# Kernel tuning notes

Measured on AMD Instinct MI355X. Metric: run time of the kernel, lower is better.

Reference implementation:

```python
import jax, jax.numpy as jnp
import numpy as np

E = 2          # n_modalities
HQ = 16        # n_heads
HK = 8         # n_kv_heads
HD = 128       # head_dim
DIM = 2048
BS = 2
SEQ = 2048
EPS = 1e-6
ROPE_THETA = 10000.0


def _rmsnorm(x, w):
    # x: (..., d), w broadcastable to x
    return x * jax.lax.rsqrt(jnp.mean(x * x, axis=-1, keepdims=True) + EPS) * w


def _apply_rope(t, cos, sin):
    # t: (bs, seq, H, HD); cos/sin: (seq, HD//2). Complex rotation on pairs.
    t2 = t.reshape(*t.shape[:-1], HD // 2, 2)
    t0, t1 = t2[..., 0], t2[..., 1]
    c = cos[None, :, None, :]
    s = sin[None, :, None, :]
    out = jnp.stack([t0 * c - t1 * s, t0 * s + t1 * c], axis=-1)
    return out.reshape(t.shape)


def setup_inputs() -> dict:
    key = jax.random.key(0)
    ks = jax.random.split(key, 8)
    pos = jnp.arange(SEQ, dtype=jnp.float32)
    inv_freq = 1.0 / (ROPE_THETA ** (jnp.arange(0, HD, 2, dtype=jnp.float32) / HD))
    ang = pos[:, None] * inv_freq[None, :]  # (SEQ, HD//2)
    return {
        "x": jax.random.normal(ks[0], (BS, SEQ, DIM), jnp.float32),
        "freqs_cos": jnp.cos(ang),
        "freqs_sin": jnp.sin(ang),
        "wq": jax.random.normal(ks[1], (E, DIM, HQ * HD), jnp.float32) * 0.02,
        "wk": jax.random.normal(ks[2], (E, DIM, HK * HD), jnp.float32) * 0.02,
        "wv": jax.random.normal(ks[3], (E, DIM, HK * HD), jnp.float32) * 0.02,
        "wo": jax.random.normal(ks[4], (E, HQ * HD, DIM), jnp.float32) * 0.02,
        "q_norm_w": jnp.ones((E, HD), jnp.float32),
        "k_norm_w": jnp.ones((E, HD), jnp.float32),
        "attn_norm_w": jnp.ones((E, DIM), jnp.float32),
        "modality_ids": jax.random.randint(ks[5], (BS * SEQ,), 0, E, jnp.int32),
    }


def reference(x, freqs_cos, freqs_sin, wq, wk, wv, wo,
              q_norm_w, k_norm_w, attn_norm_w, modality_ids):
    bs, seq, dim = x.shape
    xf = x.reshape(-1, dim)  # (N, dim)
    onehot = (modality_ids[None, :] == jnp.arange(E, dtype=modality_ids.dtype)[:, None]).astype(x.dtype)  # (E, N)

    # Per-modality QKV projections + QK RMSNorm, then combine by modality id
    q = jnp.einsum('nd,edh->enh', xf, wq).reshape(E, -1, HQ, HD)
    q = _rmsnorm(q, q_norm_w[:, None, None, :])
    q = jnp.einsum('en,enhd->nhd', onehot, q).reshape(bs, seq, HQ, HD)

    k = jnp.einsum('nd,edh->enh', xf, wk).reshape(E, -1, HK, HD)
    k = _rmsnorm(k, k_norm_w[:, None, None, :])
    k = jnp.einsum('en,enhd->nhd', onehot, k).reshape(bs, seq, HK, HD)

    v = jnp.einsum('nd,edh->enh', xf, wv).reshape(E, -1, HK, HD)
    v = jnp.einsum('en,enhd->nhd', onehot, v).reshape(bs, seq, HK, HD)

    # RoPE
    q = _apply_rope(q, freqs_cos, freqs_sin)
    k = _apply_rope(k, freqs_cos, freqs_sin)

    # repeat_kv for GQA
    n_rep = HQ // HK
    k = jnp.repeat(k, n_rep, axis=2)
    v = jnp.repeat(v, n_rep, axis=2)

    # Global causal SDPA
    qh = jnp.swapaxes(q, 1, 2)  # (bs, HQ, seq, HD)
    kh = jnp.swapaxes(k, 1, 2)
    vh = jnp.swapaxes(v, 1, 2)
    scores = jnp.einsum('bhqd,bhkd->bhqk', qh, kh) / jnp.sqrt(jnp.asarray(HD, x.dtype))
    causal = jnp.tril(jnp.ones((seq, seq), dtype=bool))
    scores = jnp.where(causal[None, None], scores, jnp.asarray(-1e30, x.dtype))
    attn = jax.nn.softmax(scores, axis=-1)
    out = jnp.einsum('bhqk,bhkd->bhqd', attn, vh)
    out_flat = jnp.swapaxes(out, 1, 2).reshape(-1, HQ * HD)  # (N, HQ*HD)

    # Per-modality output projection + RMSNorm, combine
    o = jnp.einsum('nh,ehd->end', out_flat, wo)  # (E, N, dim)
    o = _rmsnorm(o, attn_norm_w[:, None, :])
    o = jnp.einsum('en,end->nd', onehot, o)
    return o.reshape(bs, seq, dim)
```

## Files before the change

### kernel.cpp

```cpp
#include <hip/hip_runtime.h>

#define E_ 2
#define HQ_ 16
#define HK_ 8
#define HD_ 128
#define DIM_ 2048
#define BS_ 2
#define SEQ_ 2048
#define NTOK 4096

typedef unsigned short ushort_t;
typedef short bf16x8 __attribute__((ext_vector_type(8)));
typedef unsigned short ushort8 __attribute__((ext_vector_type(8)));
typedef float f32x4 __attribute__((ext_vector_type(4)));

#define MFMA(a, b, c) __builtin_amdgcn_mfma_f32_16x16x32_bf16(a, b, c, 0, 0, 0)

__device__ __forceinline__ unsigned short f2bf(float f) {
  unsigned u = __builtin_bit_cast(unsigned, f);
  u = (u + 0x7FFFu + ((u >> 16) & 1u)) >> 16;
  return (unsigned short)u;
}
__device__ __forceinline__ float bf2f(unsigned short h) {
  unsigned u = ((unsigned)h) << 16;
  return __builtin_bit_cast(float, u);
}

__device__ __forceinline__ void glds16(const void* g, void* s) {
  __builtin_amdgcn_global_load_lds(
      (const __attribute__((address_space(1))) unsigned int*)g,
      (__attribute__((address_space(3))) unsigned int*)s, 16, 0, 0);
}

__global__ __launch_bounds__(1024) void build_crow(const int* __restrict__ ids,
                                                   int* __restrict__ cnt, int* __restrict__ crow) {
  __shared__ int sc[1024];
  __shared__ int total0;
  const int t = threadIdx.x;
  int id4[4];
  int c = 0;
  for (int j = 0; j < 4; j++) {
    id4[j] = ids[t * 4 + j];
    c += (id4[j] == 0);
  }
  sc[t] = c;
  __syncthreads();
  for (int off = 1; off < 1024; off <<= 1) {
    int v = sc[t];
    int add = (t >= off) ? sc[t - off] : 0;
    __syncthreads();
    sc[t] = v + add;
    __syncthreads();
  }
  if (t == 1023) total0 = sc[1023];
  __syncthreads();
  const int cnt0 = total0;
  if (t == 0) {
    cnt[0] = cnt0;
    cnt[1] = NTOK - cnt0;
  }
  int p0 = sc[t] - c;
  int r0 = 0;
  for (int j = 0; j < 4; j++) {
    int n = t * 4 + j;
    int cr;
    if (id4[j] == 0) {
      cr = p0 + r0;
      r0++;
    } else {
      cr = cnt0 + (n - (p0 + r0));
    }
    crow[n] = cr;
  }
}

__global__ __launch_bounds__(256) void convert_scatter(const float* __restrict__ x,
                                                       const int* __restrict__ crow,
                                                       ushort_t* __restrict__ xb) {
  const int token = blockIdx.x;
  const int cr = crow[token];
  const long src = (long)token * DIM_ + threadIdx.x * 8;
  const long dst = (long)cr * DIM_ + threadIdx.x * 8;
  float4 a = *(const float4*)(x + src);
  float4 b = *(const float4*)(x + src + 4);
  ushort8 o;
  o[0] = f2bf(a.x); o[1] = f2bf(a.y); o[2] = f2bf(a.z); o[3] = f2bf(a.w);
  o[4] = f2bf(b.x); o[5] = f2bf(b.y); o[6] = f2bf(b.z); o[7] = f2bf(b.w);
  *(ushort8*)(xb + dst) = o;
}

__global__ __launch_bounds__(256) void transpose_f2b(const float* __restrict__ in,
                                                     ushort_t* __restrict__ out, int K, int N,
                                                     long inE, long outE, int outBase) {
  __shared__ float tile[32][33];
  int e = blockIdx.z;
  const float* inp = in + (long)e * inE;
  ushort_t* outp = out + (long)e * outE;
  int n0 = blockIdx.x * 32, k0 = blockIdx.y * 32;
  int tx = threadIdx.x & 31, ty = threadIdx.x >> 5;
  for (int i = 0; i < 4; i++)
    tile[ty + i * 8][tx] = inp[(long)(k0 + ty + i * 8) * N + n0 + tx];
  __syncthreads();
  for (int i = 0; i < 4; i++)
    outp[(long)(outBase + n0 + ty + i * 8) * K + k0 + tx] = f2bf(tile[tx][ty + i * 8]);
}

__global__ __launch_bounds__(256) void transpose_v(const ushort_t* __restrict__ qkv,
                                                   const int* __restrict__ crow,
                                                   ushort_t* __restrict__ vt) {
  __shared__ ushort_t tile[32][34];
  int z = blockIdx.z;
  int b = z / HK_, hk = z % HK_;
  int s0 = blockIdx.x * 32, d0 = blockIdx.y * 32;
  int tx = threadIdx.x & 31, ty = threadIdx.x >> 5;
  for (int i = 0; i < 4; i++) {
    int cr = crow[b * SEQ_ + s0 + ty + i * 8];
    tile[ty + i * 8][tx] = qkv[(long)cr * 4096 + 3072 + hk * 128 + d0 + tx];
  }
  __syncthreads();
  for (int i = 0; i < 4; i++)
    vt[((long)(b * HK_ + hk) * 128 + d0 + ty + i * 8) * SEQ_ + s0 + tx] = tile[tx][ty + i * 8];
}

__global__ __launch_bounds__(512, 2) void gemm_bt_8ph(const ushort_t* __restrict__ A,
                                                      const ushort_t* __restrict__ BT,
                                                      ushort_t* __restrict__ C, int K, int Nc,
                                                      const int* __restrict__ cnt, long btE) {
  __shared__ __align__(16) char lds[131072];
  const int bm = blockIdx.x, bn = blockIdx.y, e = blockIdx.z;
  const int cnt0 = cnt[0];
  const int scnt = e ? (NTOK - cnt0) : cnt0;
  if (bm * 256 >= scnt) return;
  const int sbase = e ? cnt0 : 0;
  const ushort_t* Bte = BT + (long)e * btE;

  const int t = threadIdx.x, w = t >> 6, lane = t & 63;
  const int quad = lane >> 4, l16 = lane & 15;
  const int wr = w >> 2, wc = w & 3;
  const int nh = wc >> 1;

  const int arow0 = sbase + bm * 256;
  const int brow0 = bn * 256;

  const int srow = t >> 2;
  const int lc = ((t & 3) - (srow >> 1)) & 3;
  int ga0 = arow0 + srow;        if (ga0 > NTOK - 1) ga0 = NTOK - 1;
  int ga1 = arow0 + 128 + srow;  if (ga1 > NTOK - 1) ga1 = NTOK - 1;
  const ushort_t* sA0 = A + (long)ga0 * K + lc * 8;
  const ushort_t* sA1 = A + (long)ga1 * K + lc * 8;
  const ushort_t* sB0 = Bte + (long)(brow0 + srow) * K + lc * 8;
  const ushort_t* sB1 = Bte + (long)(brow0 + 128 + srow) * K + lc * 8;

  char* ldsw = (char*)lds + w * 1024;
  const int aoffF = wr * 16384;
  const int boffF = 32768 + nh * 16384;

  f32x4 acc[8][4];
#pragma unroll
  for (int i = 0; i < 8; i++)
#pragma unroll
    for (int j = 0; j < 4; j++) acc[i][j] = (f32x4){0.f, 0.f, 0.f, 0.f};

  bf16x8 bfr[4];

#define STAGE_A(bufbyte, ks, kk)                                              \
  glds16(sA0 + (kk) + (ks) * 32, ldsw + (bufbyte) + (0 * 2 + (ks)) * 8192);   \
  glds16(sA1 + (kk) + (ks) * 32, ldsw + (bufbyte) + (1 * 2 + (ks)) * 8192);
#define STAGE_B(bufbyte, ks, kk)                                                      \
  glds16(sB0 + (kk) + (ks) * 32, ldsw + (bufbyte) + 32768 + (0 * 2 + (ks)) * 8192);   \
  glds16(sB1 + (kk) + (ks) * 32, ldsw + (bufbyte) + 32768 + (1 * 2 + (ks)) * 8192);

#define PHASE(ks, mfh, LOADB, STG)                                                        \
  {                                                                                       \
    bf16x8 af[4];                                                                         \
    _Pragma("unroll") for (int i = 0; i < 4; i++) {                                       \
      const int r = ((mfh)*4 + i) * 16 + l16;                                             \
      af[i] = *(const bf16x8*)(Ab + (ks)*8192 + r * 64 + ((quad + (r >> 1)) & 3) * 16);   \
    }                                                                                     \
    if (LOADB) {                                                                          \
      _Pragma("unroll") for (int nf = 0; nf < 4; nf++) {                                  \
        const int r = (wc & 1) * 64 + nf * 16 + l16;                                      \
        bfr[nf] = *(const bf16x8*)(Bb + (ks)*8192 + r * 64 + ((quad + (r >> 1)) & 3) * 16); \
      }                                                                                   \
    }                                                                                     \
    STG;                                                                                  \
    __builtin_amdgcn_s_barrier();                                                         \
    asm volatile("s_waitcnt lgkmcnt(0)" ::: "memory");                                    \
    __builtin_amdgcn_sched_barrier(0);                                                    \
    __builtin_amdgcn_s_setprio(1);                                                        \
    _Pragma("unroll") for (int i = 0; i < 4; i++)                                         \
        _Pragma("unroll") for (int nf = 0; nf < 4; nf++)                                  \
            acc[(mfh)*4 + i][nf] = MFMA(af[i], bfr[nf], acc[(mfh)*4 + i][nf]);            \
    __builtin_amdgcn_s_setprio(0);                                                        \
    __builtin_amdgcn_s_barrier();                                                         \
  }

  STAGE_A(0, 0, 0);
  STAGE_B(0, 0, 0);
  STAGE_A(0, 1, 0);
  STAGE_B(0, 1, 0);
  asm volatile("s_waitcnt vmcnt(0)" ::: "memory");
  __builtin_amdgcn_s_barrier();

  const int NT = K >> 6;
  for (int kt = 0; kt < NT; kt++) {
    const int bufb = (kt & 1) << 16;
    const int nxtb = bufb ^ 65536;
    const int k1 = (kt + 1) << 6;
    const bool st = (kt + 1) < NT;
    const char* Ab = (const char*)lds + bufb + aoffF;
    const char* Bb = (const char*)lds + bufb + boffF;

    PHASE(0, 0, 1,
          if (st) { STAGE_A(nxtb, 0, k1); asm volatile("s_waitcnt vmcnt(4)" ::: "memory"); }
          else { asm volatile("s_waitcnt vmcnt(0)" ::: "memory"); })
    PHASE(0, 1, 0,
          if (st) { STAGE_B(nxtb, 0, k1); asm volatile("s_waitcnt vmcnt(4)" ::: "memory"); }
          else { asm volatile("s_waitcnt vmcnt(0)" ::: "memory"); })
    PHASE(1, 0, 1,
          if (st) { STAGE_A(nxtb, 1, k1); asm volatile("s_waitcnt vmcnt(4)" ::: "memory"); }
          else { asm volatile("s_waitcnt vmcnt(0)" ::: "memory"); })
    PHASE(1, 1, 0,
          if (st) { STAGE_B(nxtb, 1, k1); asm volatile("s_waitcnt vmcnt(4)" ::: "memory"); }
          else { asm volatile("s_waitcnt vmcnt(0)" ::: "memory"); })
  }
#undef PHASE
#undef STAGE_A
#undef STAGE_B

#pragma unroll
  for (int mf = 0; mf < 8; mf++) {
#pragma unroll
    for (int reg = 0; reg < 4; reg++) {
      const int rl = wr * 128 + mf * 16 + quad * 4 + reg;
      if (bm * 256 + rl >= scnt) continue;
      ushort_t* Cp = C + (long)(arow0 + rl) * Nc + brow0 + wc * 64 + l16;
#pragma unroll
      for (int nf = 0; nf < 4; nf++) Cp[nf * 16] = f2bf(acc[mf][nf][reg]);
    }
  }
}

__global__ __launch_bounds__(256) void fuse_rmsrope(
    const ushort_t* __restrict__ qkv, const int* __restrict__ crow, const float* __restrict__ qw,
    const float* __restrict__ kw, const float* __restrict__ fc, const float* __restrict__ fs,
    const int* __restrict__ ids, ushort_t* __restrict__ qout, ushort_t* __restrict__ kout) {
  const int token = blockIdx.x;
  const int slot = blockIdx.y * 4 + (threadIdx.x >> 6);
  const int lane = threadIdx.x & 63;
  const int b = token >> 11, s = token & 2047;
  const int e = ids[token];
  const int cr = crow[token];
  const bool isq = slot < 16;
  const int h = isq ? slot : slot - 16;
  const ushort_t* src = qkv + (long)cr * 4096 + (isq ? slot * 128 : 2048 + h * 128);
  unsigned pv = *(const unsigned*)(src + 2 * lane);
  float v0 = bf2f((unsigned short)pv), v1 = bf2f((unsigned short)(pv >> 16));
  float ss = v0 * v0 + v1 * v1;
  ss += __shfl_xor(ss, 32); ss += __shfl_xor(ss, 16); ss += __shfl_xor(ss, 8);
  ss += __shfl_xor(ss, 4);  ss += __shfl_xor(ss, 2);  ss += __shfl_xor(ss, 1);
  float r = rsqrtf(ss * (1.0f / 128.0f) + 1e-6f);
  const float* nw = (isq ? qw : kw) + e * 128;
  v0 *= r * nw[2 * lane];
  v1 *= r * nw[2 * lane + 1];
  float c = fc[s * 64 + lane], sn = fs[s * 64 + lane];
  float o0 = v0 * c - v1 * sn;
  float o1 = v0 * sn + v1 * c;
  ushort_t* dst;
  if (isq) {
    const float QS = 0.08838834764831845f * 1.4426950408889634f;
    o0 *= QS; o1 *= QS;
    dst = qout + ((long)(b * HQ_ + h) * SEQ_ + s) * 128;
  } else {
    dst = kout + ((long)(b * HK_ + h) * SEQ_ + s) * 128;
  }
  *(unsigned*)(dst + 2 * lane) = (unsigned)f2bf(o0) | ((unsigned)f2bf(o1) << 16);
}

__global__ __launch_bounds__(256, 2) void attn_kernel(const ushort_t* __restrict__ Q,
                                                      const ushort_t* __restrict__ K,
                                                      const ushort_t* __restrict__ VT,
                                                      const int* __restrict__ crow,
                                                      ushort_t* __restrict__ O) {
  __shared__ __align__(16) ushort_t Ks[2][64 * 128];
  __shared__ __align__(16) ushort_t Vs[2][128 * 64];
  __shared__ __align__(16) ushort_t Ps[4][16][72];

  const int bh = blockIdx.y;
  const int b = bh >> 4, h = bh & 15, hk = h >> 1;
  const int t = threadIdx.x, w = t >> 6, lane = t & 63;
  const int quad = lane >> 4, l16 = lane & 15;

  const ushort_t* qbase = Q + ((long)(b * HQ_ + h) * SEQ_) * HD_;
  const ushort_t* kbase = K + ((long)(b * HK_ + hk) * SEQ_) * HD_;
  const ushort_t* vtbase = VT + ((long)(b * HK_ + hk) * HD_) * SEQ_;

#define STAGEKV(bi, s0)                                                                     \
  for (int c = 0; c < 4; c++) {                                                             \
    int lin = c * 4096 + w * 1024 + lane * 16;                                              \
    int row = lin >> 8;                                                                     \
    int gc = (((lin >> 4) & 15) - row) & 15;                                                \
    glds16(kbase + (long)((s0) + row) * HD_ + gc * 8, (char*)Ks[bi] + c * 4096 + w * 1024); \
    int d = lin >> 7;                                                                       \
    int gc2 = (((lin >> 4) & 7) - d) & 7;                                                   \
    glds16(vtbase + (long)d * SEQ_ + (s0) + gc2 * 8, (char*)Vs[bi] + c * 4096 + w * 1024);  \
  }

  const f32x4 zero = {0.f, 0.f, 0.f, 0.f};

  for (int half = 0; half < 2; half++) {
    const int qi = half ? (int)blockIdx.x : 31 - (int)blockIdx.x;
    const int q0 = qi * 64;

    for (int c = 0; c < 4; c++) {
      int lin = c * 4096 + w * 1024 + lane * 16;
      int row = lin >> 8;
      int gc = (((lin >> 4) & 15) - row) & 15;
      glds16(qbase + (long)(q0 + row) * HD_ + gc * 8, (char*)Ks[0] + c * 4096 + w * 1024);
    }
    __syncthreads();
    bf16x8 qf[4];
    {
      int row = w * 16 + l16;
      for (int kk = 0; kk < 4; kk++) {
        int cl = (kk * 4 + quad + row) & 15;
        qf[kk] = *(const bf16x8*)((const char*)Ks[0] + row * 256 + cl * 16);
      }
    }
    __syncthreads();

    f32x4 oa[8];
    for (int i = 0; i < 8; i++) oa[i] = zero;
    float rs[4] = {0.f, 0.f, 0.f, 0.f};

    const int nkt = qi + 1;
    STAGEKV(0, 0);
    __syncthreads();
    int buf = 0;
    for (int kt = 0; kt < nkt; kt++) {
      const int s0 = kt * 64;
      if (kt + 1 < nkt) STAGEKV(buf ^ 1, s0 + 64);
      const char* Kb = (const char*)Ks[buf];
      const char* Vb = (const char*)Vs[buf];

      f32x4 sa[4];
      for (int cb = 0; cb < 4; cb++) {
        sa[cb] = zero;
        int n = cb * 16 + l16;
        for (int kk = 0; kk < 4; kk++) {
          int cl = (kk * 4 + quad + n) & 15;
          bf16x8 kfrag = *(const bf16x8*)(Kb + n * 256 + cl * 16);
          sa[cb] = MFMA(qf[kk], kfrag, sa[cb]);
        }
      }
      if (kt == nkt - 1) {
        for (int cb = 0; cb < 4; cb++)
          for (int r = 0; r < 4; r++)
            if (cb * 16 + l16 > q0 + w * 16 + quad * 4 + r - s0) sa[cb][r] = -1e30f;
      }
      for (int cb = 0; cb < 4; cb++)
        for (int r = 0; r < 4; r++) {
          float p = exp2f(sa[cb][r]);
          rs[r] += p;
          Ps[w][quad * 4 + r][cb * 16 + l16] = f2bf(p);
        }
      for (int kk2 = 0; kk2 < 2; kk2++) {
        bf16x8 pf = *(const bf16x8*)&Ps[w][l16][kk2 * 32 + quad * 8];
        for (int vb = 0; vb < 8; vb++) {
          int d = vb * 16 + l16;
          int cl = (kk2 * 4 + quad + d) & 7;
          bf16x8 vfrag = *(const bf16x8*)(Vb + d * 128 + cl * 16);
          oa[vb] = MFMA(pf, vfrag, oa[vb]);
        }
      }
      __syncthreads();
      buf ^= 1;
    }

    float inv[4];
    int cr4[4];
    for (int r = 0; r < 4; r++) {
      float v = rs[r];
      v += __shfl_xor(v, 1);
      v += __shfl_xor(v, 2);
      v += __shfl_xor(v, 4);
      v += __shfl_xor(v, 8);
      inv[r] = 1.0f / v;
      cr4[r] = crow[b * SEQ_ + q0 + w * 16 + quad * 4 + r];
    }
    for (int vb = 0; vb < 8; vb++)
      for (int r = 0; r < 4; r++) {
        long off = (long)cr4[r] * 2048 + h * 128 + vb * 16 + l16;
        O[off] = f2bf(oa[vb][r] * inv[r]);
      }
  }
#undef STAGEKV
}

__global__ __launch_bounds__(256) void out_rmsnorm(const ushort_t* __restrict__ o_raw,
                                                   const int* __restrict__ crow,
                                                   const float* __restrict__ wn,
                                                   const int* __restrict__ ids,
                                                   float* __restrict__ out) {
  __shared__ float red[4];
  const int token = blockIdx.x;
  const int t = threadIdx.x, w = t >> 6, lane = t & 63;
  const int e = ids[token];
  const int cr = crow[token];
  ushort8 u = *(const ushort8*)(o_raw + (long)cr * 2048 + t * 8);
  float v[8];
  float ss = 0.f;
  for (int j = 0; j < 8; j++) {
    v[j] = bf2f(u[j]);
    ss += v[j] * v[j];
  }
  ss += __shfl_xor(ss, 32); ss += __shfl_xor(ss, 16); ss += __shfl_xor(ss, 8);
  ss += __shfl_xor(ss, 4);  ss += __shfl_xor(ss, 2);  ss += __shfl_xor(ss, 1);
  if (lane == 0) red[w] = ss;
  __syncthreads();
  float tot = red[0] + red[1] + red[2] + red[3];
  float r = rsqrtf(tot * (1.0f / 2048.0f) + 1e-6f);
  const float* wp = wn + (long)e * 2048 + t * 8;
  float* op = out + (long)token * 2048 + t * 8;
  for (int j = 0; j < 8; j++) op[j] = v[j] * r * wp[j];
}

extern "C" void kernel_launch(void* const* d_in, const int* in_sizes, int n_in, void* d_out,
                              int out_size, void* d_ws, size_t ws_size, hipStream_t stream) {
  const float* x = (const float*)d_in[0];
  const float* fc = (const float*)d_in[1];
  const float* fs = (const float*)d_in[2];
  const float* wq = (const float*)d_in[3];
  const float* wk = (const float*)d_in[4];
  const float* wv = (const float*)d_in[5];
  const float* wo = (const float*)d_in[6];
  const float* qnw = (const float*)d_in[7];
  const float* knw = (const float*)d_in[8];
  const float* anw = (const float*)d_in[9];
  const int* ids = (const int*)d_in[10];
  float* out = (float*)d_out;
  char* ws = (char*)d_ws;

  ushort_t* x_bf = (ushort_t*)(ws + 0);
  ushort_t* wqkvT = (ushort_t*)(ws + (16l << 20));
  ushort_t* woT = (ushort_t*)(ws + (16l << 20));
  int* cnt = (int*)(ws + (48l << 20));
  int* crow = (int*)(ws + (48l << 20) + 64);
  ushort_t* qkvraw = (ushort_t*)(ws + (64l << 20));
  ushort_t* qfh = (ushort_t*)(ws + (96l << 20));
  ushort_t* kfh = (ushort_t*)(ws + (112l << 20));
  ushort_t* vt = (ushort_t*)(ws + (120l << 20));
  ushort_t* o_flat = x_bf;
  ushort_t* o_raw = qkvraw;

  build_crow<<<1, 1024, 0, stream>>>(ids, cnt, crow);
  convert_scatter<<<NTOK, 256, 0, stream>>>(x, crow, x_bf);
  transpose_f2b<<<dim3(64, 64, E_), 256, 0, stream>>>(wq, wqkvT, 2048, 2048, (long)2048 * 2048,
                                                      (long)4096 * 2048, 0);
  transpose_f2b<<<dim3(32, 64, E_), 256, 0, stream>>>(wk, wqkvT, 2048, 1024, (long)2048 * 1024,
                                                      (long)4096 * 2048, 2048);
  transpose_f2b<<<dim3(32, 64, E_), 256, 0, stream>>>(wv, wqkvT, 2048, 1024, (long)2048 * 1024,
                                                      (long)4096 * 2048, 3072);
  gemm_bt_8ph<<<dim3(16, 16, E_), 512, 0, stream>>>(x_bf, wqkvT, qkvraw, 2048, 4096, cnt,
                                                    (long)4096 * 2048);
  transpose_f2b<<<dim3(64, 64, E_), 256, 0, stream>>>(wo, woT, 2048, 2048, (long)2048 * 2048,
                                                      (long)2048 * 2048, 0);
  fuse_rmsrope<<<dim3(NTOK, 6), 256, 0, stream>>>(qkvraw, crow, qnw, knw, fc, fs, ids, qfh, kfh);
  transpose_v<<<dim3(64, 4, BS_ * HK_), 256, 0, stream>>>(qkvraw, crow, vt);
  attn_kernel<<<dim3(16, 32), 256, 0, stream>>>(qfh, kfh, vt, crow, o_flat);
  gemm_bt_8ph<<<dim3(16, 8, E_), 512, 0, stream>>>(o_flat, woT, o_raw, 2048, 2048, cnt,
                                                   (long)2048 * 2048);
  out_rmsnorm<<<NTOK, 256, 0, stream>>>(o_raw, crow, anw, ids, out);
}
```

Baseline: 462.9 us.

## Rework grouped GEMM: compact modality slots, 256x128 tiles, triple-buffered K=32 pipeline

The GEMM grid changes from a full 16 row-blocks per modality, many of which exit early, to 17 compacted slots that cover both modalities' rows exactly. The tile shrinks from 256x256 to 256x128 and LDS use drops to 72KB, so launch bounds allow 4 blocks per CU. The eight-phase double-buffered K=64 loop becomes a simpler triple-buffered K=32 loop with one barrier per step. Each loaded A fragment now feeds fewer MFMAs, which lowers arithmetic intensity per LDS read.

```diff
diff --git a/kernel.cpp b/kernel.cpp
--- a/kernel.cpp
+++ b/kernel.cpp
@@ -122,13 +122,16 @@
     vt[((long)(b * HK_ + hk) * 128 + d0 + ty + i * 8) * SEQ_ + s0 + tx] = tile[tx][ty + i * 8];
 }
 
-__global__ __launch_bounds__(512, 2) void gemm_bt_8ph(const ushort_t* __restrict__ A,
-                                                      const ushort_t* __restrict__ BT,
-                                                      ushort_t* __restrict__ C, int K, int Nc,
-                                                      const int* __restrict__ cnt, long btE) {
-  __shared__ __align__(16) char lds[131072];
-  const int bm = blockIdx.x, bn = blockIdx.y, e = blockIdx.z;
+__global__ __launch_bounds__(512, 4) void gemm_bt_slot(const ushort_t* __restrict__ A,
+                                                       const ushort_t* __restrict__ BT,
+                                                       ushort_t* __restrict__ C, int K, int Nc,
+                                                       const int* __restrict__ cnt, long btE) {
+  __shared__ __align__(16) char lds[73728];
   const int cnt0 = cnt[0];
+  const int nA = (cnt0 + 255) >> 8;
+  const int slot = blockIdx.x, bn = blockIdx.y;
+  const int e = (slot < nA) ? 0 : 1;
+  const int bm = e ? slot - nA : slot;
   const int scnt = e ? (NTOK - cnt0) : cnt0;
   if (bm * 256 >= scnt) return;
   const int sbase = e ? cnt0 : 0;
@@ -137,10 +140,9 @@
   const int t = threadIdx.x, w = t >> 6, lane = t & 63;
   const int quad = lane >> 4, l16 = lane & 15;
   const int wr = w >> 2, wc = w & 3;
-  const int nh = wc >> 1;
 
   const int arow0 = sbase + bm * 256;
-  const int brow0 = bn * 256;
+  const int brow0 = bn * 128;
 
   const int srow = t >> 2;
   const int lc = ((t & 3) - (srow >> 1)) & 3;
@@ -149,84 +151,58 @@
   const ushort_t* sA0 = A + (long)ga0 * K + lc * 8;
   const ushort_t* sA1 = A + (long)ga1 * K + lc * 8;
   const ushort_t* sB0 = Bte + (long)(brow0 + srow) * K + lc * 8;
-  const ushort_t* sB1 = Bte + (long)(brow0 + 128 + srow) * K + lc * 8;
-
-  char* ldsw = (char*)lds + w * 1024;
-  const int aoffF = wr * 16384;
-  const int boffF = 32768 + nh * 16384;
-
-  f32x4 acc[8][4];
-#pragma unroll
-  for (int i = 0; i < 8; i++)
-#pragma unroll
-    for (int j = 0; j < 4; j++) acc[i][j] = (f32x4){0.f, 0.f, 0.f, 0.f};
-
-  bf16x8 bfr[4];
-
-#define STAGE_A(bufbyte, ks, kk)                                              \
-  glds16(sA0 + (kk) + (ks) * 32, ldsw + (bufbyte) + (0 * 2 + (ks)) * 8192);   \
-  glds16(sA1 + (kk) + (ks) * 32, ldsw + (bufbyte) + (1 * 2 + (ks)) * 8192);
-#define STAGE_B(bufbyte, ks, kk)                                                      \
-  glds16(sB0 + (kk) + (ks) * 32, ldsw + (bufbyte) + 32768 + (0 * 2 + (ks)) * 8192);   \
-  glds16(sB1 + (kk) + (ks) * 32, ldsw + (bufbyte) + 32768 + (1 * 2 + (ks)) * 8192);
-
-#define PHASE(ks, mfh, LOADB, STG)                                                        \
-  {                                                                                       \
-    bf16x8 af[4];                                                                         \
-    _Pragma("unroll") for (int i = 0; i < 4; i++) {                                       \
-      const int r = ((mfh)*4 + i) * 16 + l16;                                             \
-      af[i] = *(const bf16x8*)(Ab + (ks)*8192 + r * 64 + ((quad + (r >> 1)) & 3) * 16);   \
-    }                                                                                     \
-    if (LOADB) {                                                                          \
-      _Pragma("unroll") for (int nf = 0; nf < 4; nf++) {                                  \
-        const int r = (wc & 1) * 64 + nf * 16 + l16;                                      \
-        bfr[nf] = *(const bf16x8*)(Bb + (ks)*8192 + r * 64 + ((quad + (r >> 1)) & 3) * 16); \
-      }                                                                                   \
-    }                                                                                     \
-    STG;                                                                                  \
-    __builtin_amdgcn_s_barrier();                                                         \
-    asm volatile("s_waitcnt lgkmcnt(0)" ::: "memory");                                    \
-    __builtin_amdgcn_sched_barrier(0);                                                    \
-    __builtin_amdgcn_s_setprio(1);                                                        \
-    _Pragma("unroll") for (int i = 0; i < 4; i++)                                         \
-        _Pragma("unroll") for (int nf = 0; nf < 4; nf++)                                  \
-            acc[(mfh)*4 + i][nf] = MFMA(af[i], bfr[nf], acc[(mfh)*4 + i][nf]);            \
-    __builtin_amdgcn_s_setprio(0);                                                        \
-    __builtin_amdgcn_s_barrier();                                                         \
-  }
-
-  STAGE_A(0, 0, 0);
-  STAGE_B(0, 0, 0);
-  STAGE_A(0, 1, 0);
-  STAGE_B(0, 1, 0);
-  asm volatile("s_waitcnt vmcnt(0)" ::: "memory");
+
+  f32x4 acc[8][2];
+#pragma unroll
+  for (int i = 0; i < 8; i++) {
+    acc[i][0] = (f32x4){0.f, 0.f, 0.f, 0.f};
+    acc[i][1] = (f32x4){0.f, 0.f, 0.f, 0.f};
+  }
+
+#define STAGE(ps, kk)                           \
+  glds16(sA0 + (kk), (ps) + w * 1024);          \
+  glds16(sA1 + (kk), (ps) + 8192 + w * 1024);   \
+  glds16(sB0 + (kk), (ps) + 16384 + w * 1024);
+
+  char* pr = lds;
+  char* pn = lds + 24576;
+  char* ps = lds + 49152;
+
+  STAGE(pr, 0);
+  STAGE(pn, 32);
+  asm volatile("s_waitcnt vmcnt(3)" ::: "memory");
   __builtin_amdgcn_s_barrier();
 
-  const int NT = K >> 6;
+  const int NT = K >> 5;
   for (int kt = 0; kt < NT; kt++) {
-    const int bufb = (kt & 1) << 16;
-    const int nxtb = bufb ^ 65536;
-    const int k1 = (kt + 1) << 6;
-    const bool st = (kt + 1) < NT;
-    const char* Ab = (const char*)lds + bufb + aoffF;
-    const char* Bb = (const char*)lds + bufb + boffF;
-
-    PHASE(0, 0, 1,
-          if (st) { STAGE_A(nxtb, 0, k1); asm volatile("s_waitcnt vmcnt(4)" ::: "memory"); }
-          else { asm volatile("s_waitcnt vmcnt(0)" ::: "memory"); })
-    PHASE(0, 1, 0,
-          if (st) { STAGE_B(nxtb, 0, k1); asm volatile("s_waitcnt vmcnt(4)" ::: "memory"); }
-          else { asm volatile("s_waitcnt vmcnt(0)" ::: "memory"); })
-    PHASE(1, 0, 1,
-          if (st) { STAGE_A(nxtb, 1, k1); asm volatile("s_waitcnt vmcnt(4)" ::: "memory"); }
-          else { asm volatile("s_waitcnt vmcnt(0)" ::: "memory"); })
-    PHASE(1, 1, 0,
-          if (st) { STAGE_B(nxtb, 1, k1); asm volatile("s_waitcnt vmcnt(4)" ::: "memory"); }
-          else { asm volatile("s_waitcnt vmcnt(0)" ::: "memory"); })
-  }
-#undef PHASE
-#undef STAGE_A
-#undef STAGE_B
+    const bool st = (kt + 2) < NT;
+    if (st) { STAGE(ps, (kt + 2) * 32); }
+    bf16x8 af[8], bfv[2];
+#pragma unroll
+    for (int mf = 0; mf < 8; mf++) {
+      const int lr = mf * 16 + l16;
+      af[mf] = *(const bf16x8*)(pr + wr * 8192 + lr * 64 + ((quad + (lr >> 1)) & 3) * 16);
+    }
+#pragma unroll
+    for (int nf = 0; nf < 2; nf++) {
+      const int c = wc * 32 + nf * 16 + l16;
+      bfv[nf] = *(const bf16x8*)(pr + 16384 + c * 64 + ((quad + (c >> 1)) & 3) * 16);
+    }
+    asm volatile("s_waitcnt lgkmcnt(0)" ::: "memory");
+    __builtin_amdgcn_sched_barrier(0);
+    __builtin_amdgcn_s_setprio(1);
+#pragma unroll
+    for (int mf = 0; mf < 8; mf++) {
+      acc[mf][0] = MFMA(af[mf], bfv[0], acc[mf][0]);
+      acc[mf][1] = MFMA(af[mf], bfv[1], acc[mf][1]);
+    }
+    __builtin_amdgcn_s_setprio(0);
+    if (st) asm volatile("s_waitcnt vmcnt(3)" ::: "memory");
+    else    asm volatile("s_waitcnt vmcnt(0)" ::: "memory");
+    __builtin_amdgcn_s_barrier();
+    char* tmp = pr; pr = pn; pn = ps; ps = tmp;
+  }
+#undef STAGE
 
 #pragma unroll
   for (int mf = 0; mf < 8; mf++) {
@@ -234,9 +210,9 @@
     for (int reg = 0; reg < 4; reg++) {
       const int rl = wr * 128 + mf * 16 + quad * 4 + reg;
       if (bm * 256 + rl >= scnt) continue;
-      ushort_t* Cp = C + (long)(arow0 + rl) * Nc + brow0 + wc * 64 + l16;
-#pragma unroll
-      for (int nf = 0; nf < 4; nf++) Cp[nf * 16] = f2bf(acc[mf][nf][reg]);
+      ushort_t* Cp = C + (long)(arow0 + rl) * Nc + brow0 + wc * 32 + l16;
+      Cp[0] = f2bf(acc[mf][0][reg]);
+      Cp[16] = f2bf(acc[mf][1][reg]);
     }
   }
 }
@@ -461,14 +437,14 @@
                                                       (long)4096 * 2048, 2048);
   transpose_f2b<<<dim3(32, 64, E_), 256, 0, stream>>>(wv, wqkvT, 2048, 1024, (long)2048 * 1024,
                                                       (long)4096 * 2048, 3072);
-  gemm_bt_8ph<<<dim3(16, 16, E_), 512, 0, stream>>>(x_bf, wqkvT, qkvraw, 2048, 4096, cnt,
-                                                    (long)4096 * 2048);
+  gemm_bt_slot<<<dim3(17, 32), 512, 0, stream>>>(x_bf, wqkvT, qkvraw, 2048, 4096, cnt,
+                                                 (long)4096 * 2048);
   transpose_f2b<<<dim3(64, 64, E_), 256, 0, stream>>>(wo, woT, 2048, 2048, (long)2048 * 2048,
                                                       (long)2048 * 2048, 0);
   fuse_rmsrope<<<dim3(NTOK, 6), 256, 0, stream>>>(qkvraw, crow, qnw, knw, fc, fs, ids, qfh, kfh);
   transpose_v<<<dim3(64, 4, BS_ * HK_), 256, 0, stream>>>(qkvraw, crow, vt);
   attn_kernel<<<dim3(16, 32), 256, 0, stream>>>(qfh, kfh, vt, crow, o_flat);
-  gemm_bt_8ph<<<dim3(16, 8, E_), 512, 0, stream>>>(o_flat, woT, o_raw, 2048, 2048, cnt,
-                                                   (long)2048 * 2048);
+  gemm_bt_slot<<<dim3(17, 16), 512, 0, stream>>>(o_flat, woT, o_raw, 2048, 2048, cnt,
+                                                 (long)2048 * 2048);
   out_rmsnorm<<<NTOK, 256, 0, stream>>>(o_raw, crow, anw, ids, out);
 }
```

Result: no change. 459.6 us (-0.7%).
